# Performance work log

Hardware: AMD Instinct MI355X
Metric: run time of the kernel (lower is better)

## Reference

```python
import jax, jax.numpy as jnp
import numpy as np

N_EMBD = 1024
N_HEAD = 16
HEAD_DIM = N_EMBD // N_HEAD
MASK_FILL = -10.0  # module uses -10, not -inf


def setup_inputs() -> dict:
    key = jax.random.key(0)
    kx, kq, kk, kv, ko = jax.random.split(key, 5)
    B, T = 4, 2048
    s = 1.0 / np.sqrt(N_EMBD)
    return {
        "x": jax.random.normal(kx, (B, T, N_EMBD), dtype=jnp.float32),
        "wq": jax.random.normal(kq, (N_EMBD, N_EMBD), dtype=jnp.float32) * s,
        "wk": jax.random.normal(kk, (N_EMBD, N_EMBD), dtype=jnp.float32) * s,
        "wv": jax.random.normal(kv, (N_EMBD, N_EMBD), dtype=jnp.float32) * s,
        "wo": jax.random.normal(ko, (N_EMBD, N_EMBD), dtype=jnp.float32) * s,
    }


def reference(x, wq, wk, wv, wo):
    B, T, C = x.shape
    # nn.Linear applies x @ W.T; weights here stored as [out, in]
    q = (x @ wq.T).reshape(B, T, N_HEAD, HEAD_DIM).transpose(0, 2, 1, 3)
    k = (x @ wk.T).reshape(B, T, N_HEAD, HEAD_DIM).transpose(0, 2, 1, 3)
    v = (x @ wv.T).reshape(B, T, N_HEAD, HEAD_DIM).transpose(0, 2, 1, 3)
    scale = 1.0 / np.sqrt(HEAD_DIM)
    att = jnp.einsum("bhqd,bhkd->bhqk", q, k) * scale  # [B,H,T,T]
    causal = jnp.tril(jnp.ones((T, T), dtype=bool))
    att = jnp.where(causal[None, None, :, :], att, MASK_FILL)
    att = jax.nn.softmax(att, axis=-1)
    y = jnp.einsum("bhqk,bhkd->bhqd", att, v)
    y = y.transpose(0, 2, 1, 3).reshape(B, T, C)
    return y @ wo.T
```

## Files before the change

### kernel.cpp

```cpp
#include <hip/hip_runtime.h>

typedef __attribute__((ext_vector_type(8))) short bf16x8;
typedef __attribute__((ext_vector_type(4))) float f32x4;

#define T_SEQ 2048
#define EXPM10 4.5399929762484854e-05f

#define WAIT_VM8 0xF78
#define WAIT_VM0 0xF70

__device__ __forceinline__ unsigned short f2bf(float f) {
    unsigned int u = __builtin_bit_cast(unsigned int, f);
    u += 0x7fffu + ((u >> 16) & 1u);
    return (unsigned short)(u >> 16);
}
__device__ __forceinline__ float bf2f(unsigned short u) {
    return __builtin_bit_cast(float, (unsigned int)u << 16);
}

__device__ __forceinline__ void async16(void* lds, const void* g) {
    __builtin_amdgcn_global_load_lds(
        (__attribute__((address_space(1))) void*)g,
        (__attribute__((address_space(3))) void*)lds, 16, 0, 0);
}

__global__ __launch_bounds__(256) void cvt_bf16(const float* __restrict__ src,
                                                unsigned short* __restrict__ dst, int n4) {
    int i = blockIdx.x * 256 + threadIdx.x;
    if (i < n4) {
        float4 v = ((const float4*)src)[i];
        ushort4 r;
        r.x = f2bf(v.x); r.y = f2bf(v.y); r.z = f2bf(v.z); r.w = f2bf(v.w);
        ((ushort4*)dst)[i] = r;
    }
}

__global__ __launch_bounds__(256) void cvt_w(const float* __restrict__ wq,
                                             const float* __restrict__ wk,
                                             const float* __restrict__ wv,
                                             const float* __restrict__ wo,
                                             unsigned short* __restrict__ wqkv,
                                             unsigned short* __restrict__ wob) {
    int which = blockIdx.x >> 10;
    int i = (blockIdx.x & 1023) * 256 + threadIdx.x;
    const float* src = which == 0 ? wq : which == 1 ? wk : which == 2 ? wv : wo;
    unsigned short* dst = which < 3 ? wqkv + (size_t)which * 1048576 : wob;
    float4 v = ((const float4*)src)[i];
    ushort4 r;
    r.x = f2bf(v.x); r.y = f2bf(v.y); r.z = f2bf(v.z); r.w = f2bf(v.w);
    ((ushort4*)dst)[i] = r;
}

__device__ __forceinline__ void gemm128_loop(const unsigned short* __restrict__ A,
                                             const unsigned short* __restrict__ B,
                                             int m0, int n0,
                                             unsigned short (*As)[8192],
                                             unsigned short (*Bs)[8192],
                                             f32x4 acc[4][4]) {
    const int K = 1024;
    int tid = threadIdx.x;
    int wave = tid >> 6, lane = tid & 63;
    int r = lane & 15, q = lane >> 4;
    int wr = wave >> 1, wc = wave & 1;

#pragma unroll
    for (int i = 0; i < 4; i++)
#pragma unroll
        for (int j = 0; j < 4; j++) acc[i][j] = (f32x4){0.f, 0.f, 0.f, 0.f};

    int srow = tid >> 3;
    int gcol = (((tid & 7) ^ (srow & 7)) << 3);
    const unsigned short* ap[4];
    const unsigned short* bp[4];
#pragma unroll
    for (int i = 0; i < 4; i++) {
        ap[i] = A + (size_t)(m0 + i * 32 + srow) * K + gcol;
        bp[i] = B + (size_t)(n0 + i * 32 + srow) * K + gcol;
    }

    int sl0 = ((q ^ (r & 7)) << 3);
    int sl1 = (((4 | q) ^ (r & 7)) << 3);
    int rA = wr * 64 + r;
    int rB = wc * 64 + r;

#pragma unroll
    for (int i = 0; i < 4; i++) async16(&As[0][i * 2048 + wave * 512], ap[i]);
#pragma unroll
    for (int i = 0; i < 4; i++) async16(&Bs[0][i * 2048 + wave * 512], bp[i]);
    __builtin_amdgcn_sched_barrier(0);

    for (int it = 0; it < 16; ++it) {
        __builtin_amdgcn_s_barrier();
        __builtin_amdgcn_sched_barrier(0);
        if (it + 1 < 16) {
            int bn = (it + 1) & 1;
            int ko = (it + 1) * 64;
#pragma unroll
            for (int i = 0; i < 4; i++) async16(&As[bn][i * 2048 + wave * 512], ap[i] + ko);
#pragma unroll
            for (int i = 0; i < 4; i++) async16(&Bs[bn][i * 2048 + wave * 512], bp[i] + ko);
            __builtin_amdgcn_sched_barrier(0);
            __builtin_amdgcn_s_waitcnt(WAIT_VM8);
        } else {
            __builtin_amdgcn_s_waitcnt(WAIT_VM0);
        }
        __builtin_amdgcn_s_barrier();
        __builtin_amdgcn_sched_barrier(0);

        int bc = it & 1;
        bf16x8 af0[4], af1[4], bf0[4], bf1[4];
#pragma unroll
        for (int mi = 0; mi < 4; mi++) {
            af0[mi] = *(const bf16x8*)&As[bc][(rA + mi * 16) * 64 + sl0];
            af1[mi] = *(const bf16x8*)&As[bc][(rA + mi * 16) * 64 + sl1];
        }
#pragma unroll
        for (int ni = 0; ni < 4; ni++) {
            bf0[ni] = *(const bf16x8*)&Bs[bc][(rB + ni * 16) * 64 + sl0];
            bf1[ni] = *(const bf16x8*)&Bs[bc][(rB + ni * 16) * 64 + sl1];
        }
        __builtin_amdgcn_s_setprio(1);
#pragma unroll
        for (int mi = 0; mi < 4; mi++)
#pragma unroll
            for (int ni = 0; ni < 4; ni++)
                acc[mi][ni] = __builtin_amdgcn_mfma_f32_16x16x32_bf16(
                    af0[mi], bf0[ni], acc[mi][ni], 0, 0, 0);
#pragma unroll
        for (int mi = 0; mi < 4; mi++)
#pragma unroll
            for (int ni = 0; ni < 4; ni++)
                acc[mi][ni] = __builtin_amdgcn_mfma_f32_16x16x32_bf16(
                    af1[mi], bf1[ni], acc[mi][ni], 0, 0, 0);
        __builtin_amdgcn_s_setprio(0);
        __builtin_amdgcn_sched_barrier(0);
    }
}

__global__ __launch_bounds__(256) void gemm_qkv(const unsigned short* __restrict__ A,
                                                const unsigned short* __restrict__ B,
                                                unsigned short* __restrict__ Qb,
                                                unsigned short* __restrict__ Kb,
                                                unsigned short* __restrict__ Vtb) {
    __shared__ unsigned short As[2][8192];
    __shared__ unsigned short Bs[2][8192];
    int id = blockIdx.x;
    int swz = (id & 7) * 192 + (id >> 3);
    int bx = swz >> 6, by = swz & 63;
    int m0 = by * 128, n0 = bx * 128;

    f32x4 acc[4][4];
    gemm128_loop(A, B, m0, n0, As, Bs, acc);

    int tid = threadIdx.x;
    int wave = tid >> 6, lane = tid & 63;
    int r = lane & 15, q = lane >> 4;
    int wr = wave >> 1, wc = wave & 1;
#pragma unroll
    for (int mi = 0; mi < 4; mi++) {
#pragma unroll
        for (int ni = 0; ni < 4; ni++) {
#pragma unroll
            for (int rr = 0; rr < 4; rr++) {
                int gm = m0 + wr * 64 + mi * 16 + q * 4 + rr;
                int gn = n0 + wc * 64 + ni * 16 + r;
                float v = acc[mi][ni][rr];
                int b = gm >> 11, t = gm & 2047;
                int sel = gn >> 10, nn = gn & 1023;
                int h = nn >> 6, d = nn & 63;
                if (sel == 0)
                    Qb[((size_t)(b * 16 + h) * 2048 + t) * 64 + d] = f2bf(v);
                else if (sel == 1)
                    Kb[((size_t)(b * 16 + h) * 2048 + t) * 64 + d] = f2bf(v);
                else
                    Vtb[((size_t)(b * 16 + h) * 64 + d) * 2048 + t] = f2bf(v);
            }
        }
    }
}

__global__ __launch_bounds__(256) void gemm_out(const unsigned short* __restrict__ A,
                                                const unsigned short* __restrict__ B,
                                                float* __restrict__ out) {
    __shared__ unsigned short As[2][8192];
    __shared__ unsigned short Bs[2][8192];
    int id = blockIdx.x;
    int swz = (id & 7) * 64 + (id >> 3);
    int bx = swz >> 6, by = swz & 63;
    int m0 = by * 128, n0 = bx * 128;

    f32x4 acc[4][4];
    gemm128_loop(A, B, m0, n0, As, Bs, acc);

    int tid = threadIdx.x;
    int wave = tid >> 6, lane = tid & 63;
    int r = lane & 15, q = lane >> 4;
    int wr = wave >> 1, wc = wave & 1;
#pragma unroll
    for (int mi = 0; mi < 4; mi++)
#pragma unroll
        for (int ni = 0; ni < 4; ni++)
#pragma unroll
            for (int rr = 0; rr < 4; rr++) {
                int gm = m0 + wr * 64 + mi * 16 + q * 4 + rr;
                int gn = n0 + wc * 64 + ni * 16 + r;
                out[(size_t)gm * 1024 + gn] = acc[mi][ni][rr];
            }
}

__global__ __launch_bounds__(256) void suffix_sv(const unsigned short* __restrict__ Vt,
                                                 float* __restrict__ SV) {
    __shared__ float bsum[32][64];
    int bh = blockIdx.x;
    int d = threadIdx.x & 63, c = threadIdx.x >> 6;
    const unsigned short* base = Vt + ((size_t)bh * 64 + d) * T_SEQ;
#pragma unroll
    for (int jj = 0; jj < 8; jj++) {
        int j = c * 8 + jj;
        float s = 0.f;
#pragma unroll
        for (int t8 = 0; t8 < 8; t8++) {
            bf16x8 v = *(const bf16x8*)(base + j * 64 + t8 * 8);
#pragma unroll
            for (int e = 0; e < 8; e++) s += bf2f((unsigned short)v[e]);
        }
        bsum[j][d] = s;
    }
    __syncthreads();
    if (threadIdx.x < 64) {
        float run = 0.f;
        for (int j = 31; j >= 0; j--) {
            run += bsum[j][d];
            SV[((size_t)bh * 32 + j) * 64 + d] = run;
        }
    }
}

#define KST 72
#define VST 72
#define PST 72
__global__ __launch_bounds__(256) void attn(const unsigned short* __restrict__ Q,
                                            const unsigned short* __restrict__ Kg,
                                            const unsigned short* __restrict__ Vt,
                                            const float* __restrict__ SV,
                                            unsigned short* __restrict__ Y) {
    __shared__ unsigned short Ks[64 * KST];
    __shared__ unsigned short Vs[64 * VST];
    __shared__ unsigned short Ps[4][16 * PST];
    int bh = blockIdx.y;
    int tid = threadIdx.x, wave = tid >> 6, lane = tid & 63;
    int r = lane & 15, qd = lane >> 4;
    int b = bh >> 4, h = bh & 15;

    int srow = tid >> 2, scol = (tid & 3) * 16;
    const unsigned short* kg = Kg + ((size_t)bh * T_SEQ + srow) * 64 + scol;
    const unsigned short* vg = Vt + ((size_t)bh * 64 + srow) * T_SEQ + scol;
    const float scale = 0.125f;

#pragma unroll
    for (int phase = 0; phase < 2; phase++) {
        int qi = phase == 0 ? 16 + (int)blockIdx.x : 15 - (int)blockIdx.x;
        int q0 = qi * 64;
        int query = q0 + wave * 16 + r;

        const unsigned short* qptr = Q + ((size_t)bh * T_SEQ + query) * 64 + qd * 8;
        bf16x8 qf0 = *(const bf16x8*)qptr;
        bf16x8 qf1 = *(const bf16x8*)(qptr + 32);

        float l_lane = 0.0f;
        f32x4 o[4];
#pragma unroll
        for (int n = 0; n < 4; n++) o[n] = (f32x4){0.f, 0.f, 0.f, 0.f};

        bf16x8 pk0 = *(const bf16x8*)(kg);
        bf16x8 pk1 = *(const bf16x8*)(kg + 8);
        bf16x8 pv0 = *(const bf16x8*)(vg);
        bf16x8 pv1 = *(const bf16x8*)(vg + 8);

        int iters = qi + 1;
        for (int it = 0; it < iters; ++it) {
            __syncthreads();
            *(bf16x8*)&Ks[srow * KST + scol]     = pk0;
            *(bf16x8*)&Ks[srow * KST + scol + 8] = pk1;
            *(bf16x8*)&Vs[srow * VST + scol]     = pv0;
            *(bf16x8*)&Vs[srow * VST + scol + 8] = pv1;
            __syncthreads();
            if (it + 1 < iters) {
                size_t kn = (size_t)(it + 1) * 64;
                pk0 = *(const bf16x8*)(kg + kn * 64);
                pk1 = *(const bf16x8*)(kg + kn * 64 + 8);
                pv0 = *(const bf16x8*)(vg + kn);
                pv1 = *(const bf16x8*)(vg + kn + 8);
            }

            int k0 = it * 64;
            f32x4 st[4];
#pragma unroll
            for (int t = 0; t < 4; t++) {
                bf16x8 kf0 = *(const bf16x8*)&Ks[(t * 16 + r) * KST + qd * 8];
                bf16x8 kf1 = *(const bf16x8*)&Ks[(t * 16 + r) * KST + 32 + qd * 8];
                st[t] = (f32x4){0.f, 0.f, 0.f, 0.f};
                st[t] = __builtin_amdgcn_mfma_f32_16x16x32_bf16(kf0, qf0, st[t], 0, 0, 0);
                st[t] = __builtin_amdgcn_mfma_f32_16x16x32_bf16(kf1, qf1, st[t], 0, 0, 0);
            }

            float p[4][4], sum = 0.f;
            bool anymask = (k0 + 63 > q0 + wave * 16);
            if (anymask) {
#pragma unroll
                for (int t = 0; t < 4; t++)
#pragma unroll
                    for (int e = 0; e < 4; e++) {
                        int kgidx = k0 + t * 16 + qd * 4 + e;
                        float pe = __expf(st[t][e] * scale);
                        p[t][e] = (kgidx <= query) ? pe : EXPM10;
                        sum += p[t][e];
                    }
            } else {
#pragma unroll
                for (int t = 0; t < 4; t++)
#pragma unroll
                    for (int e = 0; e < 4; e++) {
                        p[t][e] = __expf(st[t][e] * scale);
                        sum += p[t][e];
                    }
            }
            l_lane += sum;

#pragma unroll
            for (int t = 0; t < 4; t++) {
                ushort4 pk;
                pk.x = f2bf(p[t][0]); pk.y = f2bf(p[t][1]);
                pk.z = f2bf(p[t][2]); pk.w = f2bf(p[t][3]);
                *(ushort4*)&Ps[wave][r * PST + t * 16 + qd * 4] = pk;
            }
            __builtin_amdgcn_sched_barrier(0);

            bf16x8 pf0 = *(const bf16x8*)&Ps[wave][r * PST + qd * 8];
            bf16x8 pf1 = *(const bf16x8*)&Ps[wave][r * PST + 32 + qd * 8];
#pragma unroll
            for (int n = 0; n < 4; n++) {
                bf16x8 vf0 = *(const bf16x8*)&Vs[(n * 16 + r) * VST + qd * 8];
                bf16x8 vf1 = *(const bf16x8*)&Vs[(n * 16 + r) * VST + 32 + qd * 8];
                o[n] = __builtin_amdgcn_mfma_f32_16x16x32_bf16(vf0, pf0, o[n], 0, 0, 0);
                o[n] = __builtin_amdgcn_mfma_f32_16x16x32_bf16(vf1, pf1, o[n], 0, 0, 0);
            }
        }

        float l_i = l_lane;
        l_i += __shfl_xor(l_i, 16);
        l_i += __shfl_xor(l_i, 32);

        int j = qi + 1;
        float pm = 0.f, tail_l = 0.f;
        float sv[4][4];
#pragma unroll
        for (int n = 0; n < 4; n++)
#pragma unroll
            for (int e = 0; e < 4; e++) sv[n][e] = 0.f;
        if (j < 32) {
            pm = EXPM10;
            tail_l = (float)(T_SEQ - 64 * j) * pm;
            const float* svp = SV + ((size_t)bh * 32 + j) * 64;
#pragma unroll
            for (int n = 0; n < 4; n++) {
                float4 f = *(const float4*)(svp + n * 16 + qd * 4);
                sv[n][0] = f.x; sv[n][1] = f.y; sv[n][2] = f.z; sv[n][3] = f.w;
            }
        }
        float inv = 1.0f / (l_i + tail_l);
#pragma unroll
        for (int n = 0; n < 4; n++) {
            ushort4 yk;
            yk.x = f2bf((o[n][0] + pm * sv[n][0]) * inv);
            yk.y = f2bf((o[n][1] + pm * sv[n][1]) * inv);
            yk.z = f2bf((o[n][2] + pm * sv[n][2]) * inv);
            yk.w = f2bf((o[n][3] + pm * sv[n][3]) * inv);
            *(ushort4*)&Y[(((size_t)b * T_SEQ + query) * 16 + h) * 64 + n * 16 + qd * 4] = yk;
        }
    }
}

extern "C" void kernel_launch(void* const* d_in, const int* in_sizes, int n_in,
                              void* d_out, int out_size, void* d_ws, size_t ws_size,
                              hipStream_t stream) {
    const float* x  = (const float*)d_in[0];
    const float* wq = (const float*)d_in[1];
    const float* wk = (const float*)d_in[2];
    const float* wv = (const float*)d_in[3];
    const float* wo = (const float*)d_in[4];

    char* ws = (char*)d_ws;
    const size_t MB = 1u << 20;
    unsigned short* xb   = (unsigned short*)(ws);
    unsigned short* Qb   = (unsigned short*)(ws + 16 * MB);
    unsigned short* Kb   = (unsigned short*)(ws + 32 * MB);
    unsigned short* Vtb  = (unsigned short*)(ws + 48 * MB);
    unsigned short* wqkv = (unsigned short*)(ws + 64 * MB);
    unsigned short* wob  = (unsigned short*)(ws + 70 * MB);
    unsigned short* Yb   = xb;
    float* SVf = (float*)d_out;

    cvt_bf16<<<8192, 256, 0, stream>>>(x, xb, 2097152);
    cvt_w<<<4096, 256, 0, stream>>>(wq, wk, wv, wo, wqkv, wob);

    gemm_qkv<<<1536, 256, 0, stream>>>(xb, wqkv, Qb, Kb, Vtb);

    suffix_sv<<<64, 256, 0, stream>>>(Vtb, SVf);

    attn<<<dim3(16, 64), 256, 0, stream>>>(Qb, Kb, Vtb, SVf, Yb);

    gemm_out<<<512, 256, 0, stream>>>(Yb, wob, (float*)d_out);
}
```

Measured before the change: 306.7 us.

## Restructure GEMMs to 256x128 tiles with 512 threads and triple-buffered K32 pipeline

Both projection GEMMs now use 512-thread blocks computing 256x128 output tiles, halving the block count, and step through K in 32-wide slices instead of 64. LDS buffering goes from double to triple, with prefetch two stages ahead and one barrier-protected wait per iteration. The aim is more B-tile reuse per load and deeper latency hiding. In exchange, the L2-friendly block swizzle is dropped, each iteration does fewer MFMAs per barrier, and the epilogue mapping assumes 8 waves.

Measured after the change: 297.1 us. 3.1% less time.

```diff
diff --git a/kernel.cpp b/kernel.cpp
--- a/kernel.cpp
+++ b/kernel.cpp
@@ -6,7 +6,7 @@
 #define T_SEQ 2048
 #define EXPM10 4.5399929762484854e-05f
 
-#define WAIT_VM8 0xF78
+#define WAIT_VM3 0xF73
 #define WAIT_VM0 0xF70
 
 __device__ __forceinline__ unsigned short f2bf(float f) {
@@ -51,12 +51,12 @@
     ((ushort4*)dst)[i] = r;
 }
 
-__device__ __forceinline__ void gemm128_loop(const unsigned short* __restrict__ A,
-                                             const unsigned short* __restrict__ B,
-                                             int m0, int n0,
-                                             unsigned short (*As)[8192],
-                                             unsigned short (*Bs)[8192],
-                                             f32x4 acc[4][4]) {
+__device__ __forceinline__ void gemm_hp(const unsigned short* __restrict__ A,
+                                        const unsigned short* __restrict__ B,
+                                        int m0, int n0,
+                                        unsigned short (*As)[8192],
+                                        unsigned short (*Bs)[4096],
+                                        f32x4 acc[4][4]) {
     const int K = 1024;
     int tid = threadIdx.x;
     int wave = tid >> 6, lane = tid & 63;
@@ -68,89 +68,76 @@
 #pragma unroll
         for (int j = 0; j < 4; j++) acc[i][j] = (f32x4){0.f, 0.f, 0.f, 0.f};
 
-    int srow = tid >> 3;
-    int gcol = (((tid & 7) ^ (srow & 7)) << 3);
-    const unsigned short* ap[4];
-    const unsigned short* bp[4];
-#pragma unroll
-    for (int i = 0; i < 4; i++) {
-        ap[i] = A + (size_t)(m0 + i * 32 + srow) * K + gcol;
-        bp[i] = B + (size_t)(n0 + i * 32 + srow) * K + gcol;
-    }
-
-    int sl0 = ((q ^ (r & 7)) << 3);
-    int sl1 = (((4 | q) ^ (r & 7)) << 3);
+    int rstg = tid >> 2;
+    int gcol = (((tid & 3) ^ (rstg & 3)) << 3);
+    const unsigned short* a0 = A + (size_t)(m0 + rstg) * K + gcol;
+    const unsigned short* a1 = A + (size_t)(m0 + 128 + rstg) * K + gcol;
+    const unsigned short* b0 = B + (size_t)(n0 + rstg) * K + gcol;
+
+    int slot = ((q ^ (r & 3)) << 3);
     int rA = wr * 64 + r;
     int rB = wc * 64 + r;
 
 #pragma unroll
-    for (int i = 0; i < 4; i++) async16(&As[0][i * 2048 + wave * 512], ap[i]);
-#pragma unroll
-    for (int i = 0; i < 4; i++) async16(&Bs[0][i * 2048 + wave * 512], bp[i]);
-    __builtin_amdgcn_sched_barrier(0);
-
-    for (int it = 0; it < 16; ++it) {
+    for (int t = 0; t < 2; ++t) {
+        async16(&As[t][tid * 8], a0 + t * 32);
+        async16(&As[t][4096 + tid * 8], a1 + t * 32);
+        async16(&Bs[t][tid * 8], b0 + t * 32);
+        __builtin_amdgcn_sched_barrier(0);
+    }
+
+    int bc = 0, bn = 2;
+    for (int it = 0; it < 32; ++it) {
+        if (it < 31) __builtin_amdgcn_s_waitcnt(WAIT_VM3);
+        else         __builtin_amdgcn_s_waitcnt(WAIT_VM0);
         __builtin_amdgcn_s_barrier();
         __builtin_amdgcn_sched_barrier(0);
-        if (it + 1 < 16) {
-            int bn = (it + 1) & 1;
-            int ko = (it + 1) * 64;
-#pragma unroll
-            for (int i = 0; i < 4; i++) async16(&As[bn][i * 2048 + wave * 512], ap[i] + ko);
-#pragma unroll
-            for (int i = 0; i < 4; i++) async16(&Bs[bn][i * 2048 + wave * 512], bp[i] + ko);
-            __builtin_amdgcn_sched_barrier(0);
-            __builtin_amdgcn_s_waitcnt(WAIT_VM8);
-        } else {
-            __builtin_amdgcn_s_waitcnt(WAIT_VM0);
-        }
+
+        bf16x8 af[4], bfr[4];
+#pragma unroll
+        for (int mi = 0; mi < 4; mi++)
+            af[mi] = *(const bf16x8*)&As[bc][(rA + mi * 16) * 32 + slot];
+#pragma unroll
+        for (int ni = 0; ni < 4; ni++)
+            bfr[ni] = *(const bf16x8*)&Bs[bc][(rB + ni * 16) * 32 + slot];
+        if (it + 2 < 32) {
+            int ko = (it + 2) * 32;
+            async16(&As[bn][tid * 8], a0 + ko);
+            async16(&As[bn][4096 + tid * 8], a1 + ko);
+            async16(&Bs[bn][tid * 8], b0 + ko);
+        }
+        __builtin_amdgcn_sched_barrier(0);
         __builtin_amdgcn_s_barrier();
         __builtin_amdgcn_sched_barrier(0);
 
-        int bc = it & 1;
-        bf16x8 af0[4], af1[4], bf0[4], bf1[4];
-#pragma unroll
-        for (int mi = 0; mi < 4; mi++) {
-            af0[mi] = *(const bf16x8*)&As[bc][(rA + mi * 16) * 64 + sl0];
-            af1[mi] = *(const bf16x8*)&As[bc][(rA + mi * 16) * 64 + sl1];
-        }
-#pragma unroll
-        for (int ni = 0; ni < 4; ni++) {
-            bf0[ni] = *(const bf16x8*)&Bs[bc][(rB + ni * 16) * 64 + sl0];
-            bf1[ni] = *(const bf16x8*)&Bs[bc][(rB + ni * 16) * 64 + sl1];
-        }
         __builtin_amdgcn_s_setprio(1);
 #pragma unroll
         for (int mi = 0; mi < 4; mi++)
 #pragma unroll
             for (int ni = 0; ni < 4; ni++)
                 acc[mi][ni] = __builtin_amdgcn_mfma_f32_16x16x32_bf16(
-                    af0[mi], bf0[ni], acc[mi][ni], 0, 0, 0);
-#pragma unroll
-        for (int mi = 0; mi < 4; mi++)
-#pragma unroll
-            for (int ni = 0; ni < 4; ni++)
-                acc[mi][ni] = __builtin_amdgcn_mfma_f32_16x16x32_bf16(
-                    af1[mi], bf1[ni], acc[mi][ni], 0, 0, 0);
+                    af[mi], bfr[ni], acc[mi][ni], 0, 0, 0);
         __builtin_amdgcn_s_setprio(0);
         __builtin_amdgcn_sched_barrier(0);
-    }
-}
-
-__global__ __launch_bounds__(256) void gemm_qkv(const unsigned short* __restrict__ A,
-                                                const unsigned short* __restrict__ B,
-                                                unsigned short* __restrict__ Qb,
-                                                unsigned short* __restrict__ Kb,
-                                                unsigned short* __restrict__ Vtb) {
-    __shared__ unsigned short As[2][8192];
-    __shared__ unsigned short Bs[2][8192];
+
+        bc = bc == 2 ? 0 : bc + 1;
+        bn = bn == 2 ? 0 : bn + 1;
+    }
+}
+
+__global__ __launch_bounds__(512, 4) void gemm_qkv(const unsigned short* __restrict__ A,
+                                                   const unsigned short* __restrict__ B,
+                                                   unsigned short* __restrict__ Qb,
+                                                   unsigned short* __restrict__ Kb,
+                                                   unsigned short* __restrict__ Vtb) {
+    __shared__ unsigned short As[3][8192];
+    __shared__ unsigned short Bs[3][4096];
     int id = blockIdx.x;
-    int swz = (id & 7) * 192 + (id >> 3);
-    int bx = swz >> 6, by = swz & 63;
-    int m0 = by * 128, n0 = bx * 128;
+    int bx = id % 24, by = id / 24;
+    int m0 = by * 256, n0 = bx * 128;
 
     f32x4 acc[4][4];
-    gemm128_loop(A, B, m0, n0, As, Bs, acc);
+    gemm_hp(A, B, m0, n0, As, Bs, acc);
 
     int tid = threadIdx.x;
     int wave = tid >> 6, lane = tid & 63;
@@ -179,18 +166,17 @@
     }
 }
 
-__global__ __launch_bounds__(256) void gemm_out(const unsigned short* __restrict__ A,
-                                                const unsigned short* __restrict__ B,
-                                                float* __restrict__ out) {
-    __shared__ unsigned short As[2][8192];
-    __shared__ unsigned short Bs[2][8192];
+__global__ __launch_bounds__(512, 4) void gemm_out(const unsigned short* __restrict__ A,
+                                                   const unsigned short* __restrict__ B,
+                                                   float* __restrict__ out) {
+    __shared__ unsigned short As[3][8192];
+    __shared__ unsigned short Bs[3][4096];
     int id = blockIdx.x;
-    int swz = (id & 7) * 64 + (id >> 3);
-    int bx = swz >> 6, by = swz & 63;
-    int m0 = by * 128, n0 = bx * 128;
+    int bx = id & 7, by = id >> 3;
+    int m0 = by * 256, n0 = bx * 128;
 
     f32x4 acc[4][4];
-    gemm128_loop(A, B, m0, n0, As, Bs, acc);
+    gemm_hp(A, B, m0, n0, As, Bs, acc);
 
     int tid = threadIdx.x;
     int wave = tid >> 6, lane = tid & 63;
@@ -404,11 +390,11 @@
     cvt_bf16<<<8192, 256, 0, stream>>>(x, xb, 2097152);
     cvt_w<<<4096, 256, 0, stream>>>(wq, wk, wv, wo, wqkv, wob);
 
-    gemm_qkv<<<1536, 256, 0, stream>>>(xb, wqkv, Qb, Kb, Vtb);
+    gemm_qkv<<<768, 512, 0, stream>>>(xb, wqkv, Qb, Kb, Vtb);
 
     suffix_sv<<<64, 256, 0, stream>>>(Vtb, SVf);
 
     attn<<<dim3(16, 64), 256, 0, stream>>>(Qb, Kb, Vtb, SVf, Yb);
 
-    gemm_out<<<512, 256, 0, stream>>>(Yb, wob, (float*)d_out);
-}
+    gemm_out<<<256, 512, 0, stream>>>(Yb, wob, (float*)d_out);
+}
```
